# Kernel tuning notes

Hardware: AMD Instinct MI355X
Metric: run time of the kernel (lower is better)

Reference implementation:

```python
import jax, jax.numpy as jnp
import numpy as np

B, T, C, H = 32, 256, 512, 512
T_OUT = 8 * T  # fixed padded expanded length (max duration per token = 8)
ALPHA = 1.0
EPS = 1e-5


def _layer_norm(x, g, b):
    mu = jnp.mean(x, axis=-1, keepdims=True)
    var = jnp.mean(jnp.square(x - mu), axis=-1, keepdims=True)
    return (x - mu) * jax.lax.rsqrt(var + EPS) * g + b


def _conv1d_same(x, w, b):
    # x: [B,T,Cin], w: [3,Cin,Cout] -> [B,T,Cout]
    y = jax.lax.conv_general_dilated(x, w, window_strides=(1,), padding='SAME',
                                     dimension_numbers=('NWC', 'WIO', 'NWC'))
    return y + b


def setup_inputs() -> dict:
    key = jax.random.key(0)
    ks = jax.random.split(key, 8)
    s1 = 1.0 / np.sqrt(3 * C)
    s2 = 1.0 / np.sqrt(3 * H)
    return {
        'x': jax.random.normal(ks[0], (B, T, C), jnp.float32),
        'true_durations': jax.random.randint(ks[1], (B, T), 0, 8, jnp.int32),
        'W1': jax.random.normal(ks[2], (3, C, H), jnp.float32) * s1,
        'b1': jnp.zeros((H,), jnp.float32),
        'g1': jnp.ones((H,), jnp.float32),
        'beta1': jnp.zeros((H,), jnp.float32),
        'W2': jax.random.normal(ks[3], (3, H, H), jnp.float32) * s2,
        'b2': jnp.zeros((H,), jnp.float32),
        'g2': jnp.ones((H,), jnp.float32),
        'beta2': jnp.zeros((H,), jnp.float32),
        'Wl': jax.random.normal(ks[4], (H, 1), jnp.float32) * (1.0 / np.sqrt(H)),
        'bl': jnp.zeros((1,), jnp.float32),
    }


def _duration_predictor(x, W1, b1, g1, beta1, W2, b2, g2, beta2, Wl, bl):
    h = jax.nn.relu(_layer_norm(_conv1d_same(x, W1, b1), g1, beta1))
    h = jax.nn.relu(_layer_norm(_conv1d_same(h, W2, b2), g2, beta2))
    return (h @ Wl + bl)[..., 0]  # [B,T]


def _expand_by_durations(x, dur):
    # cumsum-based gather: output position t takes source token i where
    # csum[i-1] <= t < csum[i]; positions >= total length are zero-padded.
    csum = jnp.cumsum(dur, axis=-1)  # [B,T]
    pos = jnp.arange(T_OUT, dtype=csum.dtype)  # [T_OUT]
    idx = jax.vmap(lambda c: jnp.searchsorted(c, pos, side='right'))(csum)  # [B,T_OUT]
    valid = pos[None, :] < csum[:, -1:]
    idx = jnp.clip(idx, 0, dur.shape[1] - 1)
    out = jnp.take_along_axis(x, idx[..., None], axis=1)  # [B,T_OUT,C]
    return out * valid[..., None].astype(x.dtype)


def reference(x, true_durations, W1, b1, g1, beta1, W2, b2, g2, beta2, Wl, bl):
    log_lengths = _duration_predictor(x, W1, b1, g1, beta1, W2, b2, g2, beta2, Wl, bl) * ALPHA
    res = _expand_by_durations(x, true_durations)
    return res, log_lengths
```

## Files before the change

### kernel.cpp

```cpp
#include <hip/hip_runtime.h>
#include <hip/hip_bf16.h>

#define B_    32
#define T_    256
#define C_    512
#define H_    512
#define TOUT_ 2048
#define TP_   258
#define K_    1536
#define EPS_  1e-5f

typedef __attribute__((ext_vector_type(8))) short bf16x8;
typedef __attribute__((ext_vector_type(4))) float f32x4;

#define GLL16(g, l)                                                        \
  __builtin_amdgcn_global_load_lds(                                        \
      (const __attribute__((address_space(1))) void*)(g),                  \
      (__attribute__((address_space(3))) void*)(l), 16, 0, 0)

__device__ __forceinline__ void wt_convert_block(const float* __restrict__ W,
                                                 __hip_bfloat16* __restrict__ Wt,
                                                 int k0, int n0, int tid,
                                                 float* tile ) {
  const int tx = tid & 31;
  const int ty = tid >> 5;
#pragma unroll
  for (int i = 0; i < 4; ++i)
    tile[(ty * 4 + i) * 33 + tx] = W[(size_t)(k0 + ty * 4 + i) * H_ + n0 + tx];
  __syncthreads();
#pragma unroll
  for (int i = 0; i < 4; ++i)
    Wt[(size_t)(n0 + ty * 4 + i) * K_ + k0 + tx] =
        __float2bfloat16(tile[tx * 33 + ty * 4 + i]);
}

__device__ __forceinline__ void csum_block(const int* __restrict__ dur,
                                           int* __restrict__ csum,
                                           int b, int tid, int* wsum) {
  int v = dur[b * T_ + tid];
#pragma unroll
  for (int off = 1; off < 64; off <<= 1) {
    int u = __shfl_up(v, off);
    if ((tid & 63) >= off) v += u;
  }
  if ((tid & 63) == 63) wsum[tid >> 6] = v;
  __syncthreads();
  int base = 0;
#pragma unroll
  for (int j = 0; j < 4; ++j)
    if (j < (tid >> 6)) base += wsum[j];
  csum[b * T_ + tid] = v + base;
}

__device__ __forceinline__ void expand_copy_block(const float* __restrict__ X,
                                                  const int* __restrict__ csum,
                                                  float* __restrict__ res,
                                                  int u, int tid) {
  const int wave = tid >> 6, lane = tid & 63;
#pragma unroll
  for (int k = 0; k < 4; ++k) {
    const int sr = u * 16 + wave * 4 + k;
    const int b = sr >> 8, t = sr & 255;
    const int* cb = csum + b * T_;
    const int c0 = t ? cb[t - 1] : 0;
    const int d  = cb[t] - c0;
    if (d == 0) continue;
    const float* src = X + (size_t)sr * C_;
    const float4 v0 = *(const float4*)(src + lane * 4);
    const float4 v1 = *(const float4*)(src + 256 + lane * 4);
    float* dst = res + ((size_t)b * TOUT_ + c0) * C_;
    for (int j = 0; j < d; ++j) {
      *(float4*)(dst + (size_t)j * C_ + lane * 4)       = v0;
      *(float4*)(dst + (size_t)j * C_ + 256 + lane * 4) = v1;
    }
  }
}

__device__ __forceinline__ void expand_zero_block(const int* __restrict__ csum,
                                                  float* __restrict__ res,
                                                  int z, int tid) {
  const int b  = z >> 6;
  const int t0 = (z & 63) << 5;
  const int total = csum[b * T_ + 255];
  const float4 z4 = make_float4(0.f, 0.f, 0.f, 0.f);
  const int half = tid >> 7, c4 = tid & 127;
#pragma unroll
  for (int rr = half; rr < 32; rr += 2) {
    const int r = t0 + rr;
    if (r >= total)
      *(float4*)(res + ((size_t)b * TOUT_ + r) * C_ + c4 * 4) = z4;
  }
}

__global__ __launch_bounds__(256) void prep_kernel(const float* __restrict__ X,
                                                   const float* __restrict__ W1,
                                                   const int* __restrict__ dur,
                                                   __hip_bfloat16* __restrict__ xpad,
                                                   __hip_bfloat16* __restrict__ hpad,
                                                   __hip_bfloat16* __restrict__ Wt1,
                                                   int* __restrict__ csum) {
  __shared__ float tile[32 * 33];
  const int tid = threadIdx.x;
  if (blockIdx.x >= 4896) {
    csum_block(dur, csum, blockIdx.x - 4896, tid, (int*)tile);
    return;
  }
  if (blockIdx.x >= 4128) {
    const int id = blockIdx.x - 4128;
    wt_convert_block(W1, Wt1, (id % 48) * 32, (id / 48) * 32, tid, tile);
    return;
  }
  const int row = blockIdx.x * 2 + (tid >> 7);
  const int b = row / TP_;
  const int t = row - b * TP_;
  const int c = (tid & 127) * 4;
  __hip_bfloat16* dst = xpad + (size_t)row * C_ + c;
  if (t == 0 || t == TP_ - 1) {
    ushort4 zz = make_ushort4(0, 0, 0, 0);
    *(ushort4*)dst = zz;
    *(ushort4*)(hpad + (size_t)row * C_ + c) = zz;
    return;
  }
  const float4 v = *(const float4*)(X + (size_t)(b * T_ + t - 1) * C_ + c);
  union { __hip_bfloat16 h[4]; ushort4 u; } o;
  o.h[0] = __float2bfloat16(v.x);
  o.h[1] = __float2bfloat16(v.y);
  o.h[2] = __float2bfloat16(v.z);
  o.h[3] = __float2bfloat16(v.w);
  *(ushort4*)dst = o.u;
}

__global__ __launch_bounds__(256) void conv_expand_kernel(
    const __hip_bfloat16* __restrict__ Apad,
    const __hip_bfloat16* __restrict__ Wt,
    const float* __restrict__ bias,
    float* __restrict__ Y,
    const float* __restrict__ X,
    const int* __restrict__ csum,
    float* __restrict__ res,
    const float* __restrict__ W2,
    __hip_bfloat16* __restrict__ Wt2,
    int ex_base) {
  __shared__ __hip_bfloat16 smA[2][2][2048];
  __shared__ __hip_bfloat16 smB[2][2][4096];

  const int tid = threadIdx.x;

  if (blockIdx.x >= 1792) {
    const int id = blockIdx.x - 1792;
    wt_convert_block(W2, Wt2, (id % 48) * 32, (id / 48) * 32, tid, (float*)smA);
    return;
  }
  if (blockIdx.x >= 512) {
    const int u = ex_base + (blockIdx.x - 512);
    if (u < 512) expand_copy_block(X, csum, res, u, tid);
    else         expand_zero_block(csum, res, u - 512, tid);
    return;
  }

  const int lane = tid & 63;
  const int wid  = tid >> 6;
  const int cid  = blockIdx.x;
  const int n0 = (cid & 3) << 7;
  const int m0 = (cid >> 2) << 6;
  const int b  = m0 >> 8;
  const int t0 = m0 & 255;
  const int wn = wid << 5;

  const int rowA  = tid >> 2;
  const int gswA  = ((tid & 3) + rowA) & 3;
  const __hip_bfloat16* arowA = Apad + (size_t)(b * TP_ + t0 + rowA) * C_ + (gswA << 3);
  const int rowB  = tid >> 2;
  const int gswB  = ((tid & 3) + rowB) & 3;
  const __hip_bfloat16* browB0 = Wt + (size_t)(n0 + rowB) * K_ + (gswB << 3);
  const __hip_bfloat16* browB1 = Wt + (size_t)(n0 + rowB + 64) * K_ + (gswB << 3);

  f32x4 acc[4][2] = {};

  auto stage = [&](int buf, int k0) {
    const int kw = k0 >> 9;
    const int c0 = k0 & 511;
    const __hip_bfloat16* a0 = arowA + kw * C_ + c0;
    GLL16(a0,      &smA[buf][0][tid << 3]);
    GLL16(a0 + 32, &smA[buf][1][tid << 3]);
    GLL16(browB0 + k0,      &smB[buf][0][tid << 3]);
    GLL16(browB1 + k0,      &smB[buf][0][(tid << 3) + 2048]);
    GLL16(browB0 + k0 + 32, &smB[buf][1][tid << 3]);
    GLL16(browB1 + k0 + 32, &smB[buf][1][(tid << 3) + 2048]);
  };

  auto compute = [&](int buf) {
    const int g   = lane >> 4;
    const int r15 = lane & 15;
    const int sa  = ((g - r15) & 3) << 3;
#pragma unroll
    for (int sl = 0; sl < 2; ++sl) {
      const __hip_bfloat16* As = smA[buf][sl];
      const __hip_bfloat16* Bs = smB[buf][sl];
      bf16x8 aF[4], bF[2];
#pragma unroll
      for (int i = 0; i < 4; ++i)
        aF[i] = *(const bf16x8*)(As + (((i << 4) + r15) << 5) + sa);
#pragma unroll
      for (int i = 0; i < 2; ++i)
        bF[i] = *(const bf16x8*)(Bs + ((wn + (i << 4) + r15) << 5) + sa);
#pragma unroll
      for (int mi = 0; mi < 4; ++mi)
#pragma unroll
        for (int ni = 0; ni < 2; ++ni)
          acc[mi][ni] = __builtin_amdgcn_mfma_f32_16x16x32_bf16(
              aF[mi], bF[ni], acc[mi][ni], 0, 0, 0);
    }
  };

  asm volatile("s_waitcnt vmcnt(0)" ::: "memory");
  stage(0, 0);
  stage(1, 64);

  for (int s = 0; s < 22; ++s) {
    asm volatile("s_waitcnt vmcnt(6)" ::: "memory");
    __builtin_amdgcn_sched_barrier(0);
    __builtin_amdgcn_s_barrier();
    compute(s & 1);
    asm volatile("s_waitcnt lgkmcnt(0)" ::: "memory");
    __builtin_amdgcn_s_barrier();
    stage(s & 1, (s + 2) << 6);
  }
  asm volatile("s_waitcnt vmcnt(6)" ::: "memory");
  __builtin_amdgcn_sched_barrier(0);
  __builtin_amdgcn_s_barrier();
  compute(0);
  asm volatile("s_waitcnt vmcnt(0)" ::: "memory");
  __builtin_amdgcn_sched_barrier(0);
  __builtin_amdgcn_s_barrier();
  compute(1);

  const int cn_base = n0 + wn + (lane & 15);
  const int rm_base = m0 + ((lane >> 4) << 2);
#pragma unroll
  for (int ni = 0; ni < 2; ++ni) {
    const int cn = cn_base + (ni << 4);
    const float bb = bias[cn];
#pragma unroll
    for (int mi = 0; mi < 4; ++mi) {
#pragma unroll
      for (int rq = 0; rq < 4; ++rq) {
        const int rm = rm_base + (mi << 4) + rq;
        Y[(size_t)rm * H_ + cn] = acc[mi][ni][rq] + bb;
      }
    }
  }
}

__global__ __launch_bounds__(256) void ln_relu_pad_kernel(const float* __restrict__ in,
                                                          const float* __restrict__ g,
                                                          const float* __restrict__ beta,
                                                          __hip_bfloat16* __restrict__ outpad) {
  const int wave = threadIdx.x >> 6;
  const int lane = threadIdx.x & 63;
  const int row  = blockIdx.x * 4 + wave;
  const float* r = in + (size_t)row * H_;

  const float4 v0 = *(const float4*)(r + lane * 4);
  const float4 v1 = *(const float4*)(r + 256 + lane * 4);

  float s = v0.x + v0.y + v0.z + v0.w + v1.x + v1.y + v1.z + v1.w;
  float q = v0.x * v0.x + v0.y * v0.y + v0.z * v0.z + v0.w * v0.w +
            v1.x * v1.x + v1.y * v1.y + v1.z * v1.z + v1.w * v1.w;
#pragma unroll
  for (int off = 32; off; off >>= 1) {
    s += __shfl_xor(s, off);
    q += __shfl_xor(q, off);
  }
  const float mu  = s * (1.0f / 512.0f);
  const float var = q * (1.0f / 512.0f) - mu * mu;
  const float rs  = rsqrtf(var + EPS_);

  const float4 g0 = *(const float4*)(g + lane * 4);
  const float4 g1 = *(const float4*)(g + 256 + lane * 4);
  const float4 e0 = *(const float4*)(beta + lane * 4);
  const float4 e1 = *(const float4*)(beta + 256 + lane * 4);

  union { __hip_bfloat16 h[4]; ushort4 u; } o0, o1;
  o0.h[0] = __float2bfloat16(fmaxf(0.f, (v0.x - mu) * rs * g0.x + e0.x));
  o0.h[1] = __float2bfloat16(fmaxf(0.f, (v0.y - mu) * rs * g0.y + e0.y));
  o0.h[2] = __float2bfloat16(fmaxf(0.f, (v0.z - mu) * rs * g0.z + e0.z));
  o0.h[3] = __float2bfloat16(fmaxf(0.f, (v0.w - mu) * rs * g0.w + e0.w));
  o1.h[0] = __float2bfloat16(fmaxf(0.f, (v1.x - mu) * rs * g1.x + e1.x));
  o1.h[1] = __float2bfloat16(fmaxf(0.f, (v1.y - mu) * rs * g1.y + e1.y));
  o1.h[2] = __float2bfloat16(fmaxf(0.f, (v1.z - mu) * rs * g1.z + e1.z));
  o1.h[3] = __float2bfloat16(fmaxf(0.f, (v1.w - mu) * rs * g1.w + e1.w));

  const int bq = row >> 8, t = row & 255;
  __hip_bfloat16* w = outpad + (size_t)(bq * TP_ + t + 1) * H_;
  *(ushort4*)(w + lane * 4)       = o0.u;
  *(ushort4*)(w + 256 + lane * 4) = o1.u;
}

__global__ __launch_bounds__(256) void ln_relu_linear_kernel(const float* __restrict__ in,
                                                             const float* __restrict__ g,
                                                             const float* __restrict__ beta,
                                                             const float* __restrict__ Wl,
                                                             const float* __restrict__ bl,
                                                             float* __restrict__ out) {
  const int wave = threadIdx.x >> 6;
  const int lane = threadIdx.x & 63;
  const int row  = blockIdx.x * 4 + wave;
  const float* r = in + (size_t)row * H_;

  const float4 v0 = *(const float4*)(r + lane * 4);
  const float4 v1 = *(const float4*)(r + 256 + lane * 4);

  float s = v0.x + v0.y + v0.z + v0.w + v1.x + v1.y + v1.z + v1.w;
  float q = v0.x * v0.x + v0.y * v0.y + v0.z * v0.z + v0.w * v0.w +
            v1.x * v1.x + v1.y * v1.y + v1.z * v1.z + v1.w * v1.w;
#pragma unroll
  for (int off = 32; off; off >>= 1) {
    s += __shfl_xor(s, off);
    q += __shfl_xor(q, off);
  }
  const float mu  = s * (1.0f / 512.0f);
  const float var = q * (1.0f / 512.0f) - mu * mu;
  const float rs  = rsqrtf(var + EPS_);

  const float4 g0 = *(const float4*)(g + lane * 4);
  const float4 g1 = *(const float4*)(g + 256 + lane * 4);
  const float4 e0 = *(const float4*)(beta + lane * 4);
  const float4 e1 = *(const float4*)(beta + 256 + lane * 4);
  const float4 w0 = *(const float4*)(Wl + lane * 4);
  const float4 w1 = *(const float4*)(Wl + 256 + lane * 4);

  float sd = 0.f;
  sd += fmaxf(0.f, (v0.x - mu) * rs * g0.x + e0.x) * w0.x;
  sd += fmaxf(0.f, (v0.y - mu) * rs * g0.y + e0.y) * w0.y;
  sd += fmaxf(0.f, (v0.z - mu) * rs * g0.z + e0.z) * w0.z;
  sd += fmaxf(0.f, (v0.w - mu) * rs * g0.w + e0.w) * w0.w;
  sd += fmaxf(0.f, (v1.x - mu) * rs * g1.x + e1.x) * w1.x;
  sd += fmaxf(0.f, (v1.y - mu) * rs * g1.y + e1.y) * w1.y;
  sd += fmaxf(0.f, (v1.z - mu) * rs * g1.z + e1.z) * w1.z;
  sd += fmaxf(0.f, (v1.w - mu) * rs * g1.w + e1.w) * w1.w;
#pragma unroll
  for (int off = 32; off; off >>= 1) sd += __shfl_xor(sd, off);

  if (lane == 0) out[row] = sd + bl[0];
}

extern "C" void kernel_launch(void* const* d_in, const int* in_sizes, int n_in,
                              void* d_out, int out_size, void* d_ws, size_t ws_size,
                              hipStream_t stream) {
  const float* x     = (const float*)d_in[0];
  const int*   dur   = (const int*)d_in[1];
  const float* W1    = (const float*)d_in[2];
  const float* b1    = (const float*)d_in[3];
  const float* g1    = (const float*)d_in[4];
  const float* beta1 = (const float*)d_in[5];
  const float* W2    = (const float*)d_in[6];
  const float* b2    = (const float*)d_in[7];
  const float* g2    = (const float*)d_in[8];
  const float* beta2 = (const float*)d_in[9];
  const float* Wl    = (const float*)d_in[10];
  const float* bl    = (const float*)d_in[11];

  float* out = (float*)d_out;
  float* res    = out;
  float* loglen = out + (size_t)B_ * TOUT_ * C_;

  char* ws = (char*)d_ws;
  __hip_bfloat16* xpad = (__hip_bfloat16*)ws;
  __hip_bfloat16* hpad = xpad + (size_t)B_ * TP_ * C_;
  __hip_bfloat16* Wt1  = hpad + (size_t)B_ * TP_ * C_;
  __hip_bfloat16* Wt2  = Wt1 + (size_t)H_ * K_;
  float* tmp1 = (float*)(Wt2 + (size_t)H_ * K_);
  int*   csum = (int*)(tmp1 + (size_t)B_ * T_ * H_);

  prep_kernel<<<4928, 256, 0, stream>>>(x, W1, dur, xpad, hpad, Wt1, csum);

  conv_expand_kernel<<<2560, 256, 0, stream>>>(xpad, Wt1, b1, tmp1,
                                               x, csum, res, W2, Wt2, 0);
  ln_relu_pad_kernel<<<B_ * T_ / 4, 256, 0, stream>>>(tmp1, g1, beta1, hpad);

  conv_expand_kernel<<<1792, 256, 0, stream>>>(hpad, Wt2, b2, tmp1,
                                               x, csum, res, nullptr, nullptr, 1280);
  ln_relu_linear_kernel<<<B_ * T_ / 4, 256, 0, stream>>>(tmp1, g2, beta2, Wl, bl, loglen);
}
```

Measured before the change: 84.50 us.

## Double GEMM tile to 128x128 with 512-thread blocks, pairing side-task work

The conv GEMM blocks move from 256 threads with a 64x128 tile to 512 threads (8 waves, a 2x4 wave grid) with a 128x128 tile, so each staged B tile is reused across twice as many rows. Each thread now issues four async global-to-LDS loads per stage instead of six, and the wait counts change to match. The expand-copy, zero-fill and weight-convert side blocks are packed two per 512-thread block, with each half using its own 256 threads and LDS region. In exchange the GEMM grid halves to 256 blocks, which may underfill the GPU's compute units, and LDS per block grows.

```diff
diff --git a/kernel.cpp b/kernel.cpp
--- a/kernel.cpp
+++ b/kernel.cpp
@@ -56,7 +56,7 @@
                                                   const int* __restrict__ csum,
                                                   float* __restrict__ res,
                                                   int u, int tid) {
-  const int wave = tid >> 6, lane = tid & 63;
+  const int wave = (tid >> 6) & 3, lane = tid & 63;
 #pragma unroll
   for (int k = 0; k < 4; ++k) {
     const int sr = u * 16 + wave * 4 + k;
@@ -83,7 +83,7 @@
   const int t0 = (z & 63) << 5;
   const int total = csum[b * T_ + 255];
   const float4 z4 = make_float4(0.f, 0.f, 0.f, 0.f);
-  const int half = tid >> 7, c4 = tid & 127;
+  const int half = (tid >> 7) & 1, c4 = tid & 127;
 #pragma unroll
   for (int rr = half; rr < 32; rr += 2) {
     const int r = t0 + rr;
@@ -130,7 +130,7 @@
   *(ushort4*)dst = o.u;
 }
 
-__global__ __launch_bounds__(256) void conv_expand_kernel(
+__global__ __launch_bounds__(512) void conv_expand_kernel(
     const __hip_bfloat16* __restrict__ Apad,
     const __hip_bfloat16* __restrict__ Wt,
     const float* __restrict__ bias,
@@ -141,20 +141,22 @@
     const float* __restrict__ W2,
     __hip_bfloat16* __restrict__ Wt2,
     int ex_base) {
-  __shared__ __hip_bfloat16 smA[2][2][2048];
+  __shared__ __hip_bfloat16 smA[2][2][4096];
   __shared__ __hip_bfloat16 smB[2][2][4096];
 
   const int tid = threadIdx.x;
 
-  if (blockIdx.x >= 1792) {
-    const int id = blockIdx.x - 1792;
-    wt_convert_block(W2, Wt2, (id % 48) * 32, (id / 48) * 32, tid, (float*)smA);
-    return;
-  }
-  if (blockIdx.x >= 512) {
-    const int u = ex_base + (blockIdx.x - 512);
-    if (u < 512) expand_copy_block(X, csum, res, u, tid);
-    else         expand_zero_block(csum, res, u - 512, tid);
+  if (blockIdx.x >= 896) {
+    const int id = (blockIdx.x - 896) * 2 + (tid >> 8);
+    float* tile = (float*)smA + (tid >> 8) * (32 * 33);
+    wt_convert_block(W2, Wt2, (id % 48) * 32, (id / 48) * 32, tid & 255, tile);
+    return;
+  }
+  if (blockIdx.x >= 256) {
+    const int u = ex_base + (blockIdx.x - 256) * 2 + (tid >> 8);
+    const int st = tid & 255;
+    if (u < 512) expand_copy_block(X, csum, res, u, st);
+    else         expand_zero_block(csum, res, u - 512, st);
     return;
   }
 
@@ -162,18 +164,16 @@
   const int wid  = tid >> 6;
   const int cid  = blockIdx.x;
   const int n0 = (cid & 3) << 7;
-  const int m0 = (cid >> 2) << 6;
+  const int m0 = (cid >> 2) << 7;
   const int b  = m0 >> 8;
   const int t0 = m0 & 255;
-  const int wn = wid << 5;
-
-  const int rowA  = tid >> 2;
-  const int gswA  = ((tid & 3) + rowA) & 3;
-  const __hip_bfloat16* arowA = Apad + (size_t)(b * TP_ + t0 + rowA) * C_ + (gswA << 3);
-  const int rowB  = tid >> 2;
-  const int gswB  = ((tid & 3) + rowB) & 3;
-  const __hip_bfloat16* browB0 = Wt + (size_t)(n0 + rowB) * K_ + (gswB << 3);
-  const __hip_bfloat16* browB1 = Wt + (size_t)(n0 + rowB + 64) * K_ + (gswB << 3);
+  const int wm = (wid >> 2) << 6;
+  const int wn = (wid & 3) << 5;
+
+  const int rowS = tid >> 2;
+  const int gsw  = ((tid & 3) + rowS) & 3;
+  const __hip_bfloat16* arowA = Apad + (size_t)(b * TP_ + t0 + rowS) * C_ + (gsw << 3);
+  const __hip_bfloat16* browB = Wt + (size_t)(n0 + rowS) * K_ + (gsw << 3);
 
   f32x4 acc[4][2] = {};
 
@@ -181,12 +181,10 @@
     const int kw = k0 >> 9;
     const int c0 = k0 & 511;
     const __hip_bfloat16* a0 = arowA + kw * C_ + c0;
-    GLL16(a0,      &smA[buf][0][tid << 3]);
-    GLL16(a0 + 32, &smA[buf][1][tid << 3]);
-    GLL16(browB0 + k0,      &smB[buf][0][tid << 3]);
-    GLL16(browB1 + k0,      &smB[buf][0][(tid << 3) + 2048]);
-    GLL16(browB0 + k0 + 32, &smB[buf][1][tid << 3]);
-    GLL16(browB1 + k0 + 32, &smB[buf][1][(tid << 3) + 2048]);
+    GLL16(a0,           &smA[buf][0][tid << 3]);
+    GLL16(a0 + 32,      &smA[buf][1][tid << 3]);
+    GLL16(browB + k0,      &smB[buf][0][tid << 3]);
+    GLL16(browB + k0 + 32, &smB[buf][1][tid << 3]);
   };
 
   auto compute = [&](int buf) {
@@ -200,7 +198,7 @@
       bf16x8 aF[4], bF[2];
 #pragma unroll
       for (int i = 0; i < 4; ++i)
-        aF[i] = *(const bf16x8*)(As + (((i << 4) + r15) << 5) + sa);
+        aF[i] = *(const bf16x8*)(As + ((wm + (i << 4) + r15) << 5) + sa);
 #pragma unroll
       for (int i = 0; i < 2; ++i)
         bF[i] = *(const bf16x8*)(Bs + ((wn + (i << 4) + r15) << 5) + sa);
@@ -218,7 +216,7 @@
   stage(1, 64);
 
   for (int s = 0; s < 22; ++s) {
-    asm volatile("s_waitcnt vmcnt(6)" ::: "memory");
+    asm volatile("s_waitcnt vmcnt(4)" ::: "memory");
     __builtin_amdgcn_sched_barrier(0);
     __builtin_amdgcn_s_barrier();
     compute(s & 1);
@@ -226,7 +224,7 @@
     __builtin_amdgcn_s_barrier();
     stage(s & 1, (s + 2) << 6);
   }
-  asm volatile("s_waitcnt vmcnt(6)" ::: "memory");
+  asm volatile("s_waitcnt vmcnt(4)" ::: "memory");
   __builtin_amdgcn_sched_barrier(0);
   __builtin_amdgcn_s_barrier();
   compute(0);
@@ -236,7 +234,7 @@
   compute(1);
 
   const int cn_base = n0 + wn + (lane & 15);
-  const int rm_base = m0 + ((lane >> 4) << 2);
+  const int rm_base = m0 + wm + ((lane >> 4) << 2);
 #pragma unroll
   for (int ni = 0; ni < 2; ++ni) {
     const int cn = cn_base + (ni << 4);
@@ -375,11 +373,11 @@
 
   prep_kernel<<<4928, 256, 0, stream>>>(x, W1, dur, xpad, hpad, Wt1, csum);
 
-  conv_expand_kernel<<<2560, 256, 0, stream>>>(xpad, Wt1, b1, tmp1,
+  conv_expand_kernel<<<1280, 512, 0, stream>>>(xpad, Wt1, b1, tmp1,
                                                x, csum, res, W2, Wt2, 0);
   ln_relu_pad_kernel<<<B_ * T_ / 4, 256, 0, stream>>>(tmp1, g1, beta1, hpad);
 
-  conv_expand_kernel<<<1792, 256, 0, stream>>>(hpad, Wt2, b2, tmp1,
-                                               x, csum, res, nullptr, nullptr, 1280);
+  conv_expand_kernel<<<896, 512, 0, stream>>>(hpad, Wt2, b2, tmp1,
+                                              x, csum, res, nullptr, nullptr, 1280);
   ln_relu_linear_kernel<<<B_ * T_ / 4, 256, 0, stream>>>(tmp1, g2, beta2, Wl, bl, loglen);
 }
```

New measurement: 82.60 us. 1.02x faster.
